# Performance work log

Hardware: AMD Instinct MI355X
Metric: run time of the kernel (lower is better)

Reference implementation:

```python
import jax, jax.numpy as jnp
import numpy as np

N_STATES = 2048
N_LABELS = 32
BATCH = 32768
LOG_CLAMP = -100.0  # torch BCELoss clamps log terms at -100


def setup_inputs() -> dict:
    key = jax.random.key(0)
    k1, k2, k3, k4 = jax.random.split(key, 4)
    f = jax.random.normal(k1, (BATCH, N_LABELS), dtype=jnp.float32)
    y = jax.random.bernoulli(k2, 0.5, (BATCH, N_LABELS)).astype(jnp.float32)
    mask = jax.random.bernoulli(k3, 0.8, (BATCH, N_LABELS)).astype(jnp.float32)
    # legal_state: binary matrix of legal label configurations (HEX graph states)
    S = jax.random.bernoulli(k4, 0.5, (N_STATES, N_LABELS)).astype(jnp.float32)
    S = S.at[0].set(1.0)  # ensure every label column has >=1 legal state
    return {"f": f, "y": y, "mask": mask, "S": S}


def reference(f, y, mask, S):
    # potential[s, b] = sum_l S[s, l] * f[b, l]
    potential = S @ f.T                      # [n_states, batch]
    max_sf = jnp.max(potential, axis=0)      # [batch]
    J = jnp.exp(potential - max_sf)          # [n_states, batch]
    z = jnp.sum(J, axis=0)                   # [batch]
    # pMargin[b, i] = sum_{s: S[s,i]>0} J[s, b] / z[b]; S is binary, so a matmul
    pMargin = (J.T @ S) / z[:, None]         # [batch, n_labels]
    # per-column BCE, masked, mean over batch, summed over columns
    log_p = jnp.maximum(jnp.log(pMargin), LOG_CLAMP)
    log_1p = jnp.maximum(jnp.log1p(-pMargin), LOG_CLAMP)
    bce = -(y * log_p + (1.0 - y) * log_1p)  # [batch, n_labels]
    loss = jnp.sum(jnp.mean(bce * mask, axis=0))
    return loss, pMargin
```

## Files before the change

kernel.cpp:

```cpp
#include <hip/hip_runtime.h>
#include <hip/hip_bf16.h>

#define NS      2048
#define NL      32
#define BATCH   32768
#define BT      64
#define NTHREADS 512
#define NCH     8

typedef __attribute__((ext_vector_type(8))) short bf16x8;
typedef __attribute__((ext_vector_type(4))) float f32x4;
typedef unsigned int u32;
typedef unsigned short u16;

__device__ inline u16 f2bf(float x) {
    union { float f; u32 u; } v; v.f = x;
    u32 r = v.u + 0x7fffu + ((v.u >> 16) & 1u);
    return (u16)(r >> 16);
}
__device__ inline u32 pk2(float a, float b) {
    return (u32)f2bf(a) | ((u32)f2bf(b) << 16);
}
__device__ inline u32 cvtpk(float a, float b) {
    u32 r;
    asm("v_cvt_pk_bf16_f32 %0, %1, %2" : "=v"(r) : "v"(a), "v"(b));
    return r;
}
__device__ inline bf16x8 frag_of(u32 w0, u32 w1, u32 w2, u32 w3) {
    union { uint4 u; bf16x8 v; } t;
    t.u = make_uint4(w0, w1, w2, w3);
    return t.v;
}
__device__ inline bf16x8 frag_of4(uint4 u) {
    union { uint4 u; bf16x8 v; } t; t.u = u; return t.v;
}

__global__ __launch_bounds__(256) void ploss_prep(
    const float* __restrict__ S, u16* __restrict__ SAp, u16* __restrict__ SBp)
{
    const int gid  = blockIdx.x * 256 + threadIdx.x;
    const int lane = gid & 63;
    const int idx  = gid >> 6;
    const int li   = lane & 15, lg = lane >> 4;

    {
        const float* r = S + (size_t)(idx * 16 + li) * NL + 4 * lg;
        float4 a = *reinterpret_cast<const float4*>(r);
        float4 c = *reinterpret_cast<const float4*>(r + 16);
        uint4 o = make_uint4(pk2(a.x, a.y), pk2(a.z, a.w),
                             pk2(c.x, c.y), pk2(c.z, c.w));
        *reinterpret_cast<uint4*>(SAp + (size_t)gid * 8) = o;
    }
    {
        const int c = idx >> 1, n = idx & 1;
        const int col = n * 16 + li;
        const float* b0 = S + (size_t)(c * 32 + 4 * lg) * NL + col;
        const float* b1 = b0 + 16 * NL;
        float v0 = b0[0 * NL], v1 = b0[1 * NL], v2 = b0[2 * NL], v3 = b0[3 * NL];
        float v4 = b1[0 * NL], v5 = b1[1 * NL], v6 = b1[2 * NL], v7 = b1[3 * NL];
        uint4 o = make_uint4(pk2(v0, v1), pk2(v2, v3), pk2(v4, v5), pk2(v6, v7));
        *reinterpret_cast<uint4*>(SBp + (size_t)gid * 8) = o;
    }
}

__global__ __launch_bounds__(NTHREADS, 4) void ploss_main(
    const float* __restrict__ f, const float* __restrict__ y,
    const float* __restrict__ msk,
    const u16* __restrict__ SAp, const u16* __restrict__ SBp,
    float* __restrict__ out, float* __restrict__ lossp)
{
    __shared__ float redbuf[8][BT][NL + 1];
    __shared__ float zbuf[8][BT];
    __shared__ float lred[8];

    const int tid  = threadIdx.x;
    const int lane = tid & 63;
    const int w    = tid >> 6;
    const int li   = lane & 15, lg = lane >> 4;
    const int b0   = blockIdx.x * BT;

    bf16x8 ffrag[4];
    #pragma unroll
    for (int nt = 0; nt < 4; ++nt) {
        const float* fr = f + (size_t)(b0 + nt * 16 + li) * NL + 4 * lg;
        float4 a = *reinterpret_cast<const float4*>(fr);
        float4 c = *reinterpret_cast<const float4*>(fr + 16);
        ffrag[nt] = frag_of(pk2(a.x, a.y), pk2(a.z, a.w),
                            pk2(c.x, c.y), pk2(c.z, c.w));
    }

    f32x4 pnum[4][2];
    #pragma unroll
    for (int nt = 0; nt < 4; ++nt)
        #pragma unroll
        for (int n2 = 0; n2 < 2; ++n2)
            pnum[nt][n2] = (f32x4){0.f, 0.f, 0.f, 0.f};
    float zp[4] = {0.f, 0.f, 0.f, 0.f};

    const u16* sa_base = SAp + (size_t)(w * NCH) * 1024;
    const u16* sb_base = SBp + (size_t)(w * NCH) * 1024;

    #pragma unroll 2
    for (int ch = 0; ch < NCH; ++ch) {
        const u16* sa = sa_base + ch * 1024;
        const u16* sb = sb_base + ch * 1024;
        bf16x8 sa0 = frag_of4(*reinterpret_cast<const uint4*>(sa + lane * 8));
        bf16x8 sa1 = frag_of4(*reinterpret_cast<const uint4*>(sa + 512 + lane * 8));
        bf16x8 sb0 = frag_of4(*reinterpret_cast<const uint4*>(sb + lane * 8));
        bf16x8 sb1 = frag_of4(*reinterpret_cast<const uint4*>(sb + 512 + lane * 8));

        bf16x8 jf[4];
        #pragma unroll
        for (int nt = 0; nt < 4; ++nt) {
            f32x4 p0 = __builtin_amdgcn_mfma_f32_16x16x32_bf16(
                sa0, ffrag[nt], (f32x4){0.f, 0.f, 0.f, 0.f}, 0, 0, 0);
            f32x4 p1 = __builtin_amdgcn_mfma_f32_16x16x32_bf16(
                sa1, ffrag[nt], (f32x4){0.f, 0.f, 0.f, 0.f}, 0, 0, 0);
            float j00 = __expf(p0[0]), j01 = __expf(p0[1]);
            float j02 = __expf(p0[2]), j03 = __expf(p0[3]);
            float j10 = __expf(p1[0]), j11 = __expf(p1[1]);
            float j12 = __expf(p1[2]), j13 = __expf(p1[3]);
            zp[nt] += ((j00 + j01) + (j02 + j03)) + ((j10 + j11) + (j12 + j13));
            jf[nt] = frag_of(cvtpk(j00, j01), cvtpk(j02, j03),
                             cvtpk(j10, j11), cvtpk(j12, j13));
        }
        #pragma unroll
        for (int nt = 0; nt < 4; ++nt) {
            pnum[nt][0] = __builtin_amdgcn_mfma_f32_16x16x32_bf16(
                jf[nt], sb0, pnum[nt][0], 0, 0, 0);
            pnum[nt][1] = __builtin_amdgcn_mfma_f32_16x16x32_bf16(
                jf[nt], sb1, pnum[nt][1], 0, 0, 0);
        }
    }

    #pragma unroll
    for (int nt = 0; nt < 4; ++nt) {
        float v = zp[nt];
        v += __shfl_xor(v, 16, 64);
        v += __shfl_xor(v, 32, 64);
        zp[nt] = v;
    }
    if (lg == 0) {
        #pragma unroll
        for (int nt = 0; nt < 4; ++nt) zbuf[w][nt * 16 + li] = zp[nt];
    }
    #pragma unroll
    for (int nt = 0; nt < 4; ++nt)
        #pragma unroll
        for (int n2 = 0; n2 < 2; ++n2)
            #pragma unroll
            for (int r = 0; r < 4; ++r)
                redbuf[w][nt * 16 + 4 * lg + r][n2 * 16 + li] = pnum[nt][n2][r];
    __syncthreads();

    const int bl = tid >> 3;
    const int l0 = (tid & 7) * 4;
    const int bg = b0 + bl;

    float zt = 0.f;
    #pragma unroll
    for (int ww = 0; ww < 8; ++ww) zt += zbuf[ww][bl];
    const float invz = 1.0f / zt;

    const float4 yv = *reinterpret_cast<const float4*>(y   + (size_t)bg * NL + l0);
    const float4 mv = *reinterpret_cast<const float4*>(msk + (size_t)bg * NL + l0);
    const float yl[4] = {yv.x, yv.y, yv.z, yv.w};
    const float ml[4] = {mv.x, mv.y, mv.z, mv.w};

    float lacc = 0.f;
    #pragma unroll
    for (int j = 0; j < 4; ++j) {
        float num = 0.f;
        #pragma unroll
        for (int ww = 0; ww < 8; ++ww) num += redbuf[ww][bl][l0 + j];
        const float p  = num * invz;
        const float om = (zt - num) * invz;
        const float lp  = fmaxf(__logf(p), -100.f);
        const float l1p = (om > 0.f) ? fmaxf(__logf(om), -100.f) : -100.f;
        const float bce = -(yl[j] * lp + (1.f - yl[j]) * l1p);
        lacc = fmaf(bce, ml[j], lacc);
        out[1 + (size_t)bg * NL + l0 + j] = p;
    }

    #pragma unroll
    for (int off = 32; off > 0; off >>= 1)
        lacc += __shfl_down(lacc, off, 64);
    if (lane == 0) lred[w] = lacc;
    __syncthreads();
    if (tid == 0) {
        float s = 0.f;
        #pragma unroll
        for (int ww = 0; ww < 8; ++ww) s += lred[ww];
        lossp[blockIdx.x] = s;
    }
}

__global__ __launch_bounds__(512) void ploss_reduce(
    const float* __restrict__ lossp, float* __restrict__ out, int nblocks)
{
    __shared__ float sdata[8];
    const int tid  = threadIdx.x;
    const int lane = tid & 63;
    const int w    = tid >> 6;
    float v = (tid < nblocks) ? lossp[tid] : 0.f;
    #pragma unroll
    for (int off = 32; off > 0; off >>= 1)
        v += __shfl_down(v, off, 64);
    if (lane == 0) sdata[w] = v;
    __syncthreads();
    if (tid == 0) {
        float s = 0.f;
        #pragma unroll
        for (int ww = 0; ww < 8; ++ww) s += sdata[ww];
        out[0] = s * (1.0f / (float)BATCH);
    }
}

extern "C" void kernel_launch(void* const* d_in, const int* in_sizes, int n_in,
                              void* d_out, int out_size, void* d_ws, size_t ws_size,
                              hipStream_t stream) {
    (void)in_sizes; (void)n_in; (void)out_size; (void)ws_size;
    const float* f   = (const float*)d_in[0];
    const float* y   = (const float*)d_in[1];
    const float* msk = (const float*)d_in[2];
    const float* S   = (const float*)d_in[3];
    float* out = (float*)d_out;

    unsigned char* ws = (unsigned char*)d_ws;
    u16* SAp     = (u16*)(ws);
    u16* SBp     = (u16*)(ws + 131072);
    float* lossp = (float*)(ws + 262144);

    ploss_prep<<<32, 256, 0, stream>>>(S, SAp, SBp);
    ploss_main<<<BATCH / BT, NTHREADS, 0, stream>>>(f, y, msk, SAp, SBp, out, lossp);
    ploss_reduce<<<1, 512, 0, stream>>>(lossp, out, BATCH / BT);
}
```

Baseline: 29.07 us.

## Fuse final loss reduction into main kernel via last-block counter; use exp2

Result: slower. 39.73 us (+36.7%).

```diff
diff --git a/kernel.cpp b/kernel.cpp
--- a/kernel.cpp
+++ b/kernel.cpp
@@ -7,12 +7,15 @@
 #define BT      64
 #define NTHREADS 512
 #define NCH     8
+#define NBLOCKS (BATCH / BT)
 
 typedef __attribute__((ext_vector_type(8))) short bf16x8;
 typedef __attribute__((ext_vector_type(4))) float f32x4;
 typedef unsigned int u32;
 typedef unsigned short u16;
 
+#define LOG2E 1.4426950408889634f
+
 __device__ inline u16 f2bf(float x) {
     union { float f; u32 u; } v; v.f = x;
     u32 r = v.u + 0x7fffu + ((v.u >> 16) & 1u);
@@ -34,14 +37,24 @@
 __device__ inline bf16x8 frag_of4(uint4 u) {
     union { uint4 u; bf16x8 v; } t; t.u = u; return t.v;
 }
+__device__ inline float exp2_hw(float x) {
+#if __has_builtin(__builtin_amdgcn_exp2f)
+    return __builtin_amdgcn_exp2f(x);
+#else
+    return exp2f(x);
+#endif
+}
 
 __global__ __launch_bounds__(256) void ploss_prep(
-    const float* __restrict__ S, u16* __restrict__ SAp, u16* __restrict__ SBp)
+    const float* __restrict__ S, u16* __restrict__ SAp, u16* __restrict__ SBp,
+    u32* __restrict__ cnt)
 {
     const int gid  = blockIdx.x * 256 + threadIdx.x;
     const int lane = gid & 63;
     const int idx  = gid >> 6;
     const int li   = lane & 15, lg = lane >> 4;
+
+    if (gid == 0) *cnt = 0u;
 
     {
         const float* r = S + (size_t)(idx * 16 + li) * NL + 4 * lg;
@@ -67,11 +80,12 @@
     const float* __restrict__ f, const float* __restrict__ y,
     const float* __restrict__ msk,
     const u16* __restrict__ SAp, const u16* __restrict__ SBp,
-    float* __restrict__ out, float* __restrict__ lossp)
+    float* __restrict__ out, float* __restrict__ lossp, u32* __restrict__ cnt)
 {
     __shared__ float redbuf[8][BT][NL + 1];
     __shared__ float zbuf[8][BT];
     __shared__ float lred[8];
+    __shared__ u32 isLast;
 
     const int tid  = threadIdx.x;
     const int lane = tid & 63;
@@ -85,8 +99,10 @@
         const float* fr = f + (size_t)(b0 + nt * 16 + li) * NL + 4 * lg;
         float4 a = *reinterpret_cast<const float4*>(fr);
         float4 c = *reinterpret_cast<const float4*>(fr + 16);
-        ffrag[nt] = frag_of(pk2(a.x, a.y), pk2(a.z, a.w),
-                            pk2(c.x, c.y), pk2(c.z, c.w));
+        ffrag[nt] = frag_of(pk2(a.x * LOG2E, a.y * LOG2E),
+                            pk2(a.z * LOG2E, a.w * LOG2E),
+                            pk2(c.x * LOG2E, c.y * LOG2E),
+                            pk2(c.z * LOG2E, c.w * LOG2E));
     }
 
     f32x4 pnum[4][2];
@@ -116,10 +132,10 @@
                 sa0, ffrag[nt], (f32x4){0.f, 0.f, 0.f, 0.f}, 0, 0, 0);
             f32x4 p1 = __builtin_amdgcn_mfma_f32_16x16x32_bf16(
                 sa1, ffrag[nt], (f32x4){0.f, 0.f, 0.f, 0.f}, 0, 0, 0);
-            float j00 = __expf(p0[0]), j01 = __expf(p0[1]);
-            float j02 = __expf(p0[2]), j03 = __expf(p0[3]);
-            float j10 = __expf(p1[0]), j11 = __expf(p1[1]);
-            float j12 = __expf(p1[2]), j13 = __expf(p1[3]);
+            float j00 = exp2_hw(p0[0]), j01 = exp2_hw(p0[1]);
+            float j02 = exp2_hw(p0[2]), j03 = exp2_hw(p0[3]);
+            float j10 = exp2_hw(p1[0]), j11 = exp2_hw(p1[1]);
+            float j12 = exp2_hw(p1[2]), j13 = exp2_hw(p1[3]);
             zp[nt] += ((j00 + j01) + (j02 + j03)) + ((j10 + j11) + (j12 + j13));
             jf[nt] = frag_of(cvtpk(j00, j01), cvtpk(j02, j03),
                              cvtpk(j10, j11), cvtpk(j12, j13));
@@ -187,32 +203,31 @@
         lacc += __shfl_down(lacc, off, 64);
     if (lane == 0) lred[w] = lacc;
     __syncthreads();
+
     if (tid == 0) {
         float s = 0.f;
         #pragma unroll
         for (int ww = 0; ww < 8; ++ww) s += lred[ww];
-        lossp[blockIdx.x] = s;
-    }
-}
-
-__global__ __launch_bounds__(512) void ploss_reduce(
-    const float* __restrict__ lossp, float* __restrict__ out, int nblocks)
-{
-    __shared__ float sdata[8];
-    const int tid  = threadIdx.x;
-    const int lane = tid & 63;
-    const int w    = tid >> 6;
-    float v = (tid < nblocks) ? lossp[tid] : 0.f;
-    #pragma unroll
-    for (int off = 32; off > 0; off >>= 1)
-        v += __shfl_down(v, off, 64);
-    if (lane == 0) sdata[w] = v;
+        atomicExch(&lossp[blockIdx.x], s);
+        __threadfence();
+        u32 old = atomicAdd(cnt, 1u);
+        isLast = (old == (u32)(NBLOCKS - 1)) ? 1u : 0u;
+    }
     __syncthreads();
-    if (tid == 0) {
-        float s = 0.f;
-        #pragma unroll
-        for (int ww = 0; ww < 8; ++ww) s += sdata[ww];
-        out[0] = s * (1.0f / (float)BATCH);
+    if (isLast) {
+        __threadfence();
+        float v = atomicAdd(&lossp[tid], 0.0f);
+        #pragma unroll
+        for (int off = 32; off > 0; off >>= 1)
+            v += __shfl_down(v, off, 64);
+        if (lane == 0) lred[w] = v;
+        __syncthreads();
+        if (tid == 0) {
+            float s = 0.f;
+            #pragma unroll
+            for (int ww = 0; ww < 8; ++ww) s += lred[ww];
+            out[0] = s * (1.0f / (float)BATCH);
+        }
     }
 }
 
@@ -230,8 +245,8 @@
     u16* SAp     = (u16*)(ws);
     u16* SBp     = (u16*)(ws + 131072);
     float* lossp = (float*)(ws + 262144);
-
-    ploss_prep<<<32, 256, 0, stream>>>(S, SAp, SBp);
-    ploss_main<<<BATCH / BT, NTHREADS, 0, stream>>>(f, y, msk, SAp, SBp, out, lossp);
-    ploss_reduce<<<1, 512, 0, stream>>>(lossp, out, BATCH / BT);
-}
+    u32*   cnt   = (u32*)(ws + 264192);
+
+    ploss_prep<<<32, 256, 0, stream>>>(S, SAp, SBp, cnt);
+    ploss_main<<<NBLOCKS, NTHREADS, 0, stream>>>(f, y, msk, SAp, SBp, out, lossp, cnt);
+}
```

## Halve LDS reduction buffer with two-pass epilogue and use exp2 with prescaled inputs

Applied to the files above, without the earlier changes.

New measurement: 28.44 us (median of 3 runs). 1.02x faster.

```diff
diff --git a/kernel.cpp b/kernel.cpp
--- a/kernel.cpp
+++ b/kernel.cpp
@@ -7,12 +7,15 @@
 #define BT      64
 #define NTHREADS 512
 #define NCH     8
+#define NBLOCKS (BATCH / BT)
 
 typedef __attribute__((ext_vector_type(8))) short bf16x8;
 typedef __attribute__((ext_vector_type(4))) float f32x4;
 typedef unsigned int u32;
 typedef unsigned short u16;
 
+#define LOG2E 1.4426950408889634f
+
 __device__ inline u16 f2bf(float x) {
     union { float f; u32 u; } v; v.f = x;
     u32 r = v.u + 0x7fffu + ((v.u >> 16) & 1u);
@@ -33,6 +36,13 @@
 }
 __device__ inline bf16x8 frag_of4(uint4 u) {
     union { uint4 u; bf16x8 v; } t; t.u = u; return t.v;
+}
+__device__ inline float exp2_hw(float x) {
+#if __has_builtin(__builtin_amdgcn_exp2f)
+    return __builtin_amdgcn_exp2f(x);
+#else
+    return exp2f(x);
+#endif
 }
 
 __global__ __launch_bounds__(256) void ploss_prep(
@@ -69,7 +79,7 @@
     const u16* __restrict__ SAp, const u16* __restrict__ SBp,
     float* __restrict__ out, float* __restrict__ lossp)
 {
-    __shared__ float redbuf[8][BT][NL + 1];
+    __shared__ float redbuf[8][BT][17];
     __shared__ float zbuf[8][BT];
     __shared__ float lred[8];
 
@@ -85,8 +95,10 @@
         const float* fr = f + (size_t)(b0 + nt * 16 + li) * NL + 4 * lg;
         float4 a = *reinterpret_cast<const float4*>(fr);
         float4 c = *reinterpret_cast<const float4*>(fr + 16);
-        ffrag[nt] = frag_of(pk2(a.x, a.y), pk2(a.z, a.w),
-                            pk2(c.x, c.y), pk2(c.z, c.w));
+        ffrag[nt] = frag_of(pk2(a.x * LOG2E, a.y * LOG2E),
+                            pk2(a.z * LOG2E, a.w * LOG2E),
+                            pk2(c.x * LOG2E, c.y * LOG2E),
+                            pk2(c.z * LOG2E, c.w * LOG2E));
     }
 
     f32x4 pnum[4][2];
@@ -116,10 +128,10 @@
                 sa0, ffrag[nt], (f32x4){0.f, 0.f, 0.f, 0.f}, 0, 0, 0);
             f32x4 p1 = __builtin_amdgcn_mfma_f32_16x16x32_bf16(
                 sa1, ffrag[nt], (f32x4){0.f, 0.f, 0.f, 0.f}, 0, 0, 0);
-            float j00 = __expf(p0[0]), j01 = __expf(p0[1]);
-            float j02 = __expf(p0[2]), j03 = __expf(p0[3]);
-            float j10 = __expf(p1[0]), j11 = __expf(p1[1]);
-            float j12 = __expf(p1[2]), j13 = __expf(p1[3]);
+            float j00 = exp2_hw(p0[0]), j01 = exp2_hw(p0[1]);
+            float j02 = exp2_hw(p0[2]), j03 = exp2_hw(p0[3]);
+            float j10 = exp2_hw(p1[0]), j11 = exp2_hw(p1[1]);
+            float j12 = exp2_hw(p1[2]), j13 = exp2_hw(p1[3]);
             zp[nt] += ((j00 + j01) + (j02 + j03)) + ((j10 + j11) + (j12 + j13));
             jf[nt] = frag_of(cvtpk(j00, j01), cvtpk(j02, j03),
                              cvtpk(j10, j11), cvtpk(j12, j13));
@@ -144,42 +156,73 @@
         #pragma unroll
         for (int nt = 0; nt < 4; ++nt) zbuf[w][nt * 16 + li] = zp[nt];
     }
+
     #pragma unroll
     for (int nt = 0; nt < 4; ++nt)
         #pragma unroll
-        for (int n2 = 0; n2 < 2; ++n2)
-            #pragma unroll
-            for (int r = 0; r < 4; ++r)
-                redbuf[w][nt * 16 + 4 * lg + r][n2 * 16 + li] = pnum[nt][n2][r];
+        for (int r = 0; r < 4; ++r)
+            redbuf[w][nt * 16 + 4 * lg + r][li] = pnum[nt][0][r];
     __syncthreads();
 
     const int bl = tid >> 3;
-    const int l0 = (tid & 7) * 4;
+    const int j2 = (tid & 7) * 2;
     const int bg = b0 + bl;
 
     float zt = 0.f;
     #pragma unroll
     for (int ww = 0; ww < 8; ++ww) zt += zbuf[ww][bl];
     const float invz = 1.0f / zt;
-
-    const float4 yv = *reinterpret_cast<const float4*>(y   + (size_t)bg * NL + l0);
-    const float4 mv = *reinterpret_cast<const float4*>(msk + (size_t)bg * NL + l0);
-    const float yl[4] = {yv.x, yv.y, yv.z, yv.w};
-    const float ml[4] = {mv.x, mv.y, mv.z, mv.w};
-
     float lacc = 0.f;
-    #pragma unroll
-    for (int j = 0; j < 4; ++j) {
-        float num = 0.f;
-        #pragma unroll
-        for (int ww = 0; ww < 8; ++ww) num += redbuf[ww][bl][l0 + j];
-        const float p  = num * invz;
-        const float om = (zt - num) * invz;
-        const float lp  = fmaxf(__logf(p), -100.f);
-        const float l1p = (om > 0.f) ? fmaxf(__logf(om), -100.f) : -100.f;
-        const float bce = -(yl[j] * lp + (1.f - yl[j]) * l1p);
-        lacc = fmaf(bce, ml[j], lacc);
-        out[1 + (size_t)bg * NL + l0 + j] = p;
+
+    {
+        const float2 yv = *reinterpret_cast<const float2*>(y   + (size_t)bg * NL + j2);
+        const float2 mv = *reinterpret_cast<const float2*>(msk + (size_t)bg * NL + j2);
+        float num0 = 0.f, num1 = 0.f;
+        #pragma unroll
+        for (int ww = 0; ww < 8; ++ww) {
+            num0 += redbuf[ww][bl][j2];
+            num1 += redbuf[ww][bl][j2 + 1];
+        }
+        const float pa = num0 * invz,        pb = num1 * invz;
+        const float oa = (zt - num0) * invz, ob = (zt - num1) * invz;
+        const float lpa  = fmaxf(__logf(pa), -100.f);
+        const float lpb  = fmaxf(__logf(pb), -100.f);
+        const float l1pa = (oa > 0.f) ? fmaxf(__logf(oa), -100.f) : -100.f;
+        const float l1pb = (ob > 0.f) ? fmaxf(__logf(ob), -100.f) : -100.f;
+        lacc = fmaf(-(yv.x * lpa + (1.f - yv.x) * l1pa), mv.x, lacc);
+        lacc = fmaf(-(yv.y * lpb + (1.f - yv.y) * l1pb), mv.y, lacc);
+        out[1 + (size_t)bg * NL + j2]     = pa;
+        out[1 + (size_t)bg * NL + j2 + 1] = pb;
+    }
+    __syncthreads();
+
+    #pragma unroll
+    for (int nt = 0; nt < 4; ++nt)
+        #pragma unroll
+        for (int r = 0; r < 4; ++r)
+            redbuf[w][nt * 16 + 4 * lg + r][li] = pnum[nt][1][r];
+    __syncthreads();
+
+    {
+        const int l0 = 16 + j2;
+        const float2 yv = *reinterpret_cast<const float2*>(y   + (size_t)bg * NL + l0);
+        const float2 mv = *reinterpret_cast<const float2*>(msk + (size_t)bg * NL + l0);
+        float num0 = 0.f, num1 = 0.f;
+        #pragma unroll
+        for (int ww = 0; ww < 8; ++ww) {
+            num0 += redbuf[ww][bl][j2];
+            num1 += redbuf[ww][bl][j2 + 1];
+        }
+        const float pa = num0 * invz,        pb = num1 * invz;
+        const float oa = (zt - num0) * invz, ob = (zt - num1) * invz;
+        const float lpa  = fmaxf(__logf(pa), -100.f);
+        const float lpb  = fmaxf(__logf(pb), -100.f);
+        const float l1pa = (oa > 0.f) ? fmaxf(__logf(oa), -100.f) : -100.f;
+        const float l1pb = (ob > 0.f) ? fmaxf(__logf(ob), -100.f) : -100.f;
+        lacc = fmaf(-(yv.x * lpa + (1.f - yv.x) * l1pa), mv.x, lacc);
+        lacc = fmaf(-(yv.y * lpb + (1.f - yv.y) * l1pb), mv.y, lacc);
+        out[1 + (size_t)bg * NL + l0]     = pa;
+        out[1 + (size_t)bg * NL + l0 + 1] = pb;
     }
 
     #pragma unroll
@@ -232,6 +275,6 @@
     float* lossp = (float*)(ws + 262144);
 
     ploss_prep<<<32, 256, 0, stream>>>(S, SAp, SBp);
-    ploss_main<<<BATCH / BT, NTHREADS, 0, stream>>>(f, y, msk, SAp, SBp, out, lossp);
-    ploss_reduce<<<1, 512, 0, stream>>>(lossp, out, BATCH / BT);
-}
+    ploss_main<<<NBLOCKS, NTHREADS, 0, stream>>>(f, y, msk, SAp, SBp, out, lossp);
+    ploss_reduce<<<1, 512, 0, stream>>>(lossp, out, NBLOCKS);
+}
```
